# Optimization experiments

Hardware: AMD Instinct MI355X
Metric: run time of the kernel (lower is better)

The kernel has to match this reference:

```python
import jax, jax.numpy as jnp
import numpy as np

H = 16  # head_num


def setup_inputs() -> dict:
    key = jax.random.key(0)
    ks = jax.random.split(key, 16)
    B, N, D, DR = 4, 512, 1024, 128
    dk = D // H
    nrm = lambda i, shp, sc=1.0: jax.random.normal(ks[i], shp, jnp.float32) * sc
    inp = {
        "q": nrm(0, (B, N, D)),
        "k": nrm(1, (B, N, D)),
        "v": nrm(2, (B, N, D)),
        "r_k": nrm(3, (B, N, N, DR), 0.1),
        "r_v": nrm(4, (B, N, N, DR), 0.1),
        # learned params (Linear stored as [in, out] so y = x @ W + b)
        "Wq": nrm(5, (D, D), 1.0 / np.sqrt(D)), "bq": jnp.zeros((D,), jnp.float32),
        "Wk": nrm(6, (D, D), 1.0 / np.sqrt(D)), "bk": jnp.zeros((D,), jnp.float32),
        "Wv": nrm(7, (D, D), 1.0 / np.sqrt(D)), "bv": jnp.zeros((D,), jnp.float32),
        "Wrk": nrm(8, (DR, dk), 1.0 / np.sqrt(DR)), "brk": jnp.zeros((dk,), jnp.float32),
        "Wrv": nrm(9, (DR, dk), 1.0 / np.sqrt(DR)), "brv": jnp.zeros((dk,), jnp.float32),
        "Wo": nrm(10, (D, D), 1.0 / np.sqrt(D)), "bo": jnp.zeros((D,), jnp.float32),
    }
    return inp


def reference(q, k, v, r_k, r_v, Wq, bq, Wk, bk, Wv, bv, Wrk, brk, Wrv, brv, Wo, bo):
    B, N, D = q.shape
    dk = D // H
    scale = 1.0 / np.sqrt(dk).astype(np.float32)
    # relation projections ('concat' mode, rel_share=False): [B,N,N,d_rel] -> [B,N,N,d_k]
    rk = r_k @ Wrk + brk
    rv = r_v @ Wrv + brv

    def heads(x, W, b):  # [B,N,D] -> [B,H,N,dk]
        return (x @ W + b).reshape(B, N, H, dk).transpose(0, 2, 1, 3)

    qh = heads(q, Wq, bq)
    kh = heads(k, Wk, bk)
    vh = heads(v, Wv, bv)
    # score_1: standard scaled dot-product; score_2: relation bias per (query m, key n)
    score = jnp.einsum('bhmd,bhnd->bhmn', qh, kh) * scale \
          + jnp.einsum('bhmd,bmnd->bhmn', qh, rk)
    att = jax.nn.softmax(score, axis=-1)  # [B,H,N,N]
    # value_1: standard AV; value_2: relation-value combination
    val = jnp.einsum('bhmn,bhnd->bhmd', att, vh) \
        + jnp.einsum('bhmn,bmnd->bhmd', att, rv)
    out = val.transpose(0, 2, 1, 3).reshape(B, N, D) @ Wo + bo
    return out
```

## Files before the change

kernel.cpp:

```cpp
#include <hip/hip_runtime.h>
#include <hip/hip_bf16.h>
#include <hip/hip_fp16.h>
#include <stdint.h>


typedef __attribute__((ext_vector_type(4))) float f32x4;
typedef __attribute__((ext_vector_type(8))) short s16x8;

#define MFMA16(A, B, C) __builtin_amdgcn_mfma_f32_16x16x32_bf16(A, B, C, 0, 0, 0)

__device__ __forceinline__ uint16_t f2bf(float x) {
  uint32_t u = __float_as_uint(x);
  u += 0x7fffu + ((u >> 16) & 1u);
  return (uint16_t)(u >> 16);
}
__device__ __forceinline__ float bf2f(uint16_t u) {
  return __uint_as_float((uint32_t)u << 16);
}
__device__ __forceinline__ uint16_t f2h(float x) {
  __half h = __float2half_rn(x);
  return *reinterpret_cast<uint16_t*>(&h);
}
__device__ __forceinline__ float h2f(uint16_t u) {
  __half h = *reinterpret_cast<__half*>(&u);
  return __half2float(h);
}

__device__ __forceinline__ uint32_t cvtpk(float lo, float hi) {
  uint32_t r;
  asm("v_cvt_pk_bf16_f32 %0, %1, %2" : "=v"(r) : "v"(lo), "v"(hi));
  return r;
}

__device__ __forceinline__ s16x8 pack8(float4 a, float4 b) {
  union { uint32_t u[4]; s16x8 v; } r;
  r.u[0] = cvtpk(a.x, a.y);
  r.u[1] = cvtpk(a.z, a.w);
  r.u[2] = cvtpk(b.x, b.y);
  r.u[3] = cvtpk(b.z, b.w);
  return r.v;
}

__device__ __forceinline__ void gll16(const void* g, void* l) {
  __builtin_amdgcn_global_load_lds(
      (const __attribute__((address_space(1))) uint32_t*)(g),
      (__attribute__((address_space(3))) uint32_t*)(l), 16, 0, 0);
}

__global__ __launch_bounds__(256) void k_prep(
    const float* __restrict__ Wq, const float* __restrict__ Wk,
    const float* __restrict__ Wv, const float* __restrict__ Wo,
    const float* __restrict__ Wrk, const float* __restrict__ Wrv,
    uint16_t* __restrict__ WqT, uint16_t* __restrict__ WkT,
    uint16_t* __restrict__ WvT, uint16_t* __restrict__ WoT,
    uint16_t* __restrict__ WrkB, uint16_t* __restrict__ WrvT) {
  int z = blockIdx.y;
  int t = threadIdx.x;
  if (z == 4) {
    if (blockIdx.x == 0) {
      for (int i = t; i < 128 * 64; i += 256) WrkB[i] = f2bf(Wrk[i]);
      for (int i = t; i < 64 * 128; i += 256) {
        int d = i >> 7, r = i & 127;
        WrvT[i] = f2bf(Wrv[r * 64 + d]);
      }
    }
    return;
  }
  const float* W = (z == 0) ? Wq : (z == 1) ? Wk : (z == 2) ? Wv : Wo;
  uint16_t* O = (z == 0) ? WqT : (z == 1) ? WkT : (z == 2) ? WvT : WoT;
  int tk = (blockIdx.x >> 4) * 64;
  int tn = (blockIdx.x & 15) * 64;
  __shared__ float tile[64][65];
  {
    int kk = t >> 2, c0 = (t & 3) * 16;
    const float* src = W + (size_t)(tk + kk) * 1024 + tn + c0;
#pragma unroll
    for (int i = 0; i < 16; i += 4) {
      float4 v = *(const float4*)(src + i);
      tile[kk][c0 + i + 0] = v.x; tile[kk][c0 + i + 1] = v.y;
      tile[kk][c0 + i + 2] = v.z; tile[kk][c0 + i + 3] = v.w;
    }
  }
  __syncthreads();
  {
    int n_loc = t >> 2;
    int n = tn + n_loc;
#pragma unroll
    for (int cc = 0; cc < 2; ++cc) {
      int c = (t & 3) * 2 + cc;
      int csrc = c ^ (n & 7);
      s16x8 pk;
#pragma unroll
      for (int j = 0; j < 8; ++j) pk[j] = (short)f2bf(tile[csrc * 8 + j][n_loc]);
      *reinterpret_cast<s16x8*>(O + (size_t)n * 1024 + tk + c * 8) = pk;
    }
  }
}

__global__ __launch_bounds__(256) void k_projqkv(
    const float* __restrict__ Xq, const float* __restrict__ Xk,
    const float* __restrict__ Xv, const uint16_t* __restrict__ WTbase,
    const float* __restrict__ bq, const float* __restrict__ bk,
    const float* __restrict__ bv, uint16_t* __restrict__ outbase) {
  int mode = blockIdx.z;
  const float* X = (mode == 0) ? Xq : (mode == 1) ? Xk : Xv;
  const float* bias = (mode == 0) ? bq : (mode == 1) ? bk : bv;
  const uint16_t* WT = WTbase + (size_t)mode * (1u << 20);
  uint16_t* out = outbase + (size_t)mode * (2u << 20);

  __shared__ alignas(16) float Xs[128 * 64];
  __shared__ alignas(16) uint16_t Bs[128 * 64];
  int t = threadIdx.x, lane = t & 63, w = t >> 6, lr = lane & 15, lg = lane >> 4;
  int m0 = blockIdx.x * 128, n0 = blockIdx.y * 128;
  int wm = (w >> 1) * 64, wn = (w & 1) * 64;
  f32x4 acc[4][4];
#pragma unroll
  for (int i = 0; i < 4; ++i)
#pragma unroll
    for (int j = 0; j < 4; ++j) acc[i][j] = (f32x4){0.f, 0.f, 0.f, 0.f};
  for (int ko = 0; ko < 16; ++ko) {
    __syncthreads();
    {
#pragma unroll
      for (int i = 0; i < 8; ++i) {
        int u = i * 256 + t;
        int row = u >> 4, c16 = u & 15;
        int cs = c16 ^ (row & 15);
        gll16(X + (size_t)(m0 + row) * 1024 + ko * 64 + cs * 4, (char*)Xs + u * 16);
      }
#pragma unroll
      for (int i = 0; i < 4; ++i) {
        int u = i * 256 + t;
        int row = u >> 3, c2 = u & 7;
        gll16(WT + (size_t)(n0 + row) * 1024 + ko * 64 + c2 * 8, (char*)Bs + u * 16);
      }
    }
    __syncthreads();
#pragma unroll
    for (int kk = 0; kk < 2; ++kk) {
      s16x8 af[4], bf[4];
#pragma unroll
      for (int mt = 0; mt < 4; ++mt) {
        int row = wm + mt * 16 + lr;
        int c0 = kk * 8 + lg * 2;
        float4 v0 = *(const float4*)((const char*)Xs + row * 256 +
                                     ((c0 ^ (row & 15)) * 16));
        float4 v1 = *(const float4*)((const char*)Xs + row * 256 +
                                     (((c0 + 1) ^ (row & 15)) * 16));
        af[mt] = pack8(v0, v1);
      }
#pragma unroll
      for (int nt = 0; nt < 4; ++nt) {
        int row = wn + nt * 16 + lr;
        bf[nt] = *(const s16x8*)((const char*)Bs + row * 128 +
                                 (((kk * 32 + lg * 8) * 2) ^ ((row & 7) << 4)));
      }
#pragma unroll
      for (int mt = 0; mt < 4; ++mt)
#pragma unroll
        for (int nt = 0; nt < 4; ++nt)
          acc[mt][nt] = MFMA16(af[mt], bf[nt], acc[mt][nt]);
    }
  }
  float sc = (mode == 1) ? 0.125f : 1.0f;
#pragma unroll
  for (int mt = 0; mt < 4; ++mt) {
#pragma unroll
    for (int nt = 0; nt < 4; ++nt) {
      int col = n0 + wn + nt * 16 + lr;
      float bcol = bias[col];
      if (mode != 2) {
#pragma unroll
        for (int r = 0; r < 4; ++r) {
          int row = m0 + wm + mt * 16 + lg * 4 + r;
          out[(size_t)row * 1024 + col] = f2bf((acc[mt][nt][r] + bcol) * sc);
        }
      } else {
        int row0 = m0 + wm + mt * 16 + lg * 4;
        int b = row0 >> 9, n = row0 & 511;
        int h = col >> 6, d = col & 63;
        ushort4 pk;
        pk.x = f2bf(acc[mt][nt][0] + bcol);
        pk.y = f2bf(acc[mt][nt][1] + bcol);
        pk.z = f2bf(acc[mt][nt][2] + bcol);
        pk.w = f2bf(acc[mt][nt][3] + bcol);
        *reinterpret_cast<ushort4*>(out + ((size_t)(b * 16 + h) * 64 + d) * 512 + n) = pk;
      }
    }
  }
}

__global__ __launch_bounds__(256) void k_score1qt(
    const uint16_t* __restrict__ qh, const uint16_t* __restrict__ kh,
    const uint16_t* __restrict__ WrkB, uint16_t* __restrict__ S1,
    uint16_t* __restrict__ qt) {
  __shared__ alignas(16) uint16_t Qs[128 * 64];
  __shared__ alignas(16) uint16_t Ks[2][128 * 64];
  int t = threadIdx.x, lane = t & 63, w = t >> 6, lr = lane & 15, lg = lane >> 4;
  int b = blockIdx.z;
  if (blockIdx.x >= 4) {
    int slot = (blockIdx.x - 4) * 64 + blockIdx.y * 4 + b;
#pragma unroll
    for (int it = 0; it < 4; ++it) {
      int row0 = slot * 256 + it * 64 + w * 16;
      f32x4 acc[8];
#pragma unroll
      for (int i = 0; i < 8; ++i) acc[i] = (f32x4){0.f, 0.f, 0.f, 0.f};
      s16x8 af[2];
#pragma unroll
      for (int kk = 0; kk < 2; ++kk)
        af[kk] = *(const s16x8*)(qh + (size_t)(row0 + lr) * 64 + kk * 32 + lg * 8);
#pragma unroll
      for (int rt = 0; rt < 8; ++rt) {
#pragma unroll
        for (int kk = 0; kk < 2; ++kk) {
          s16x8 bf = *(const s16x8*)(WrkB + (size_t)(rt * 16 + lr) * 64 + kk * 32 + lg * 8);
          acc[rt] = MFMA16(af[kk], bf, acc[rt]);
        }
      }
#pragma unroll
      for (int rt = 0; rt < 8; ++rt)
#pragma unroll
        for (int r = 0; r < 4; ++r)
          qt[(size_t)(row0 + lg * 4 + r) * 128 + rt * 16 + lr] = f2bf(acc[rt][r]);
    }
    return;
  }
  int mt = blockIdx.x, h = blockIdx.y;
  int m0 = mt * 128;
  const char* qg = (const char*)(qh + (size_t)(b * 512 + m0) * 1024 + h * 64);
  const char* kg = (const char*)(kh + (size_t)b * 512 * 1024 + h * 64);
#pragma unroll
  for (int i = 0; i < 4; ++i) {
    int u = i * 256 + t;
    int row = u >> 3;
    int cs = (u & 7) ^ (row & 7);
    gll16(qg + (size_t)row * 2048 + cs * 16, (char*)Qs + u * 16);
    gll16(kg + (size_t)row * 2048 + cs * 16, (char*)Ks[0] + u * 16);
  }
  int wm = (w >> 1) * 64, wn = (w & 1) * 64;
  int hsw = (h & 7) << 3;
#pragma unroll
  for (int nt = 0; nt < 4; ++nt) {
    asm volatile("s_waitcnt vmcnt(0)" ::: "memory");
    __builtin_amdgcn_s_barrier();
    asm volatile("" ::: "memory");
    if (nt < 3) {
      const char* kgn = kg + (size_t)(nt + 1) * 128 * 2048;
#pragma unroll
      for (int i = 0; i < 4; ++i) {
        int u = i * 256 + t;
        int row = u >> 3;
        int cs = (u & 7) ^ (row & 7);
        gll16(kgn + (size_t)row * 2048 + cs * 16, (char*)Ks[(nt + 1) & 1] + u * 16);
      }
    }
    f32x4 acc[4][4];
#pragma unroll
    for (int i = 0; i < 4; ++i)
#pragma unroll
      for (int j = 0; j < 4; ++j) acc[i][j] = (f32x4){0.f, 0.f, 0.f, 0.f};
#pragma unroll
    for (int kk = 0; kk < 2; ++kk) {
      s16x8 af[4], bf[4];
#pragma unroll
      for (int mtt = 0; mtt < 4; ++mtt) {
        int row = wm + mtt * 16 + lr;
        af[mtt] = *(const s16x8*)((const char*)Qs + row * 128 +
                                  (((kk * 4 + lg) ^ (row & 7)) * 16));
      }
#pragma unroll
      for (int ntt = 0; ntt < 4; ++ntt) {
        int row = wn + ntt * 16 + lr;
        bf[ntt] = *(const s16x8*)((const char*)Ks[nt & 1] + row * 128 +
                                  (((kk * 4 + lg) ^ (row & 7)) * 16));
      }
#pragma unroll
      for (int mtt = 0; mtt < 4; ++mtt)
#pragma unroll
        for (int ntt = 0; ntt < 4; ++ntt)
          acc[mtt][ntt] = MFMA16(bf[ntt], af[mtt], acc[mtt][ntt]);
    }
#pragma unroll
    for (int mtt = 0; mtt < 4; ++mtt) {
#pragma unroll
      for (int ntt = 0; ntt < 4; ++ntt) {
        int m = b * 512 + m0 + wm + mtt * 16 + lr;
        int nsw = (nt * 128 + wn + ntt * 16 + lg * 4) ^ hsw;
        ushort4 u4;
        u4.x = f2h(acc[mtt][ntt][0]); u4.y = f2h(acc[mtt][ntt][1]);
        u4.z = f2h(acc[mtt][ntt][2]); u4.w = f2h(acc[mtt][ntt][3]);
        *(ushort4*)(S1 + (size_t)m * 8192 + h * 512 + nsw) = u4;
      }
    }
  }
}

#define RKSTEP(s)                                                              \
  {                                                                            \
    asm volatile("s_waitcnt vmcnt(%0)" ::                                      \
                 "i"(((s) < 2) ? 6 : (((s) < 31) ? 2 : 0)) : "memory");        \
    const char* bp_ = wpriv + ((s) & 1) * 2048 + lr * 128;                     \
    float4 v0_ = *(const float4*)(bp_ + (((lg * 2 + 0) ^ (lr & 7)) * 16));     \
    float4 v1_ = *(const float4*)(bp_ + (((lg * 2 + 1) ^ (lr & 7)) * 16));     \
    acc[(s) >> 2] = MFMA16(aqt[(s) & 3], pack8(v0_, v1_), acc[(s) >> 2]);      \
    if ((s) + 2 < 32) {                                                        \
      const int s2_ = (s) + 2;                                                 \
      const char* src_ = rkb + (size_t)((s2_ >> 2) * 64 + w * 16 + r_lo) * 512 \
                         + (s2_ & 3) * 128 + c16s * 16;                        \
      char* dst_ = wpriv + (s2_ & 1) * 2048 + lane * 16;                       \
      gll16(src_, dst_);                                                       \
      gll16(src_ + 8 * 512, dst_ + 1024);                                      \
    }                                                                          \
  }

#define RVI(c)                                                                 \
  { _Pragma("unroll")                                                          \
    for (int i_ = 0; i_ < 2; ++i_) {                                           \
      int u_ = i_ * 64 + lane;                                                 \
      gll16(rvb + (size_t)(((c) >> 1) * 32 + (u_ >> 2)) * 512 + w * 128 +      \
                ((c) & 1) * 64 + (u_ & 3) * 16,                                \
            wpriv + ((c) & 1) * 2048 + u_ * 16);                               \
    } }

#define RVC(c, accv)                                                           \
  {                                                                            \
    s16x8 a_ = *(const s16x8*)((const char*)att_lds + lr * 1024 +              \
        (((uint32_t)(((c) >> 1) * 64 + lg * 16)) ^ ((uint32_t)(lr & 7) << 4)));\
    const float* vb_ = (const float*)(wpriv + ((c) & 1) * 2048);               \
    union { uint32_t u[4]; s16x8 v; } bb_;                                     \
    _Pragma("unroll")                                                          \
    for (int i = 0; i < 4; ++i)                                                \
      bb_.u[i] = cvtpk(vb_[(lg * 8 + 2 * i) * 16 + lr],                        \
                       vb_[(lg * 8 + 2 * i + 1) * 16 + lr]);                   \
    accv = MFMA16(a_, bb_.v, accv);                                            \
  }

__global__ __launch_bounds__(256, 4) void k_s2v2(
    const uint16_t* __restrict__ qt, const float* __restrict__ rk,
    const float* __restrict__ rv, uint16_t* SATT,
    const uint16_t* __restrict__ WrvT, const float* __restrict__ brv,
    uint16_t* __restrict__ V2) {
  int bm = blockIdx.x;
  int t = threadIdx.x, lane = t & 63, w = t >> 6, lr = lane & 15, lg = lane >> 4;
  __shared__ alignas(16) char stream_lds[16384];
  __shared__ alignas(16) uint16_t att_lds[16 * 512];
  __shared__ alignas(16) uint16_t arv_lds[16 * 128];
  __shared__ float red[2][16][4];
  char* wpriv = stream_lds + w * 4096;
  const int r_lo = lane >> 3;
  const int c16s = (lane & 7) ^ r_lo;

  s16x8 aqt[4];
#pragma unroll
  for (int kk = 0; kk < 4; ++kk)
    aqt[kk] = *(const s16x8*)(qt + ((size_t)bm * 16 + lr) * 128 + kk * 32 + lg * 8);

  const char* rkb = (const char*)(rk + (size_t)bm * 65536);
#pragma unroll
  for (int s2 = 0; s2 < 2; ++s2) {
    const char* src_ = rkb + (size_t)(w * 16 + r_lo) * 512 + s2 * 128 + c16s * 16;
    char* dst_ = wpriv + s2 * 2048 + lane * 16;
    gll16(src_, dst_);
    gll16(src_ + 8 * 512, dst_ + 1024);
  }
  const char* s1g = (const char*)(SATT + (size_t)bm * 8192);
#pragma unroll
  for (int i = 0; i < 4; ++i)
    gll16(s1g + i * 4096 + t * 16, (char*)att_lds + i * 4096 + t * 16);

  f32x4 acc[8];
#pragma unroll
  for (int j = 0; j < 8; ++j) acc[j] = (f32x4){0.f, 0.f, 0.f, 0.f};

  RKSTEP(0)  RKSTEP(1)  RKSTEP(2)  RKSTEP(3)  RKSTEP(4)  RKSTEP(5)  RKSTEP(6)  RKSTEP(7)
  RKSTEP(8)  RKSTEP(9)  RKSTEP(10) RKSTEP(11) RKSTEP(12) RKSTEP(13) RKSTEP(14) RKSTEP(15)
  RKSTEP(16) RKSTEP(17) RKSTEP(18) RKSTEP(19) RKSTEP(20) RKSTEP(21) RKSTEP(22) RKSTEP(23)
  RKSTEP(24) RKSTEP(25) RKSTEP(26) RKSTEP(27) RKSTEP(28) RKSTEP(29) RKSTEP(30) RKSTEP(31)

  __syncthreads();

  const char* rvb = (const char*)(rv + (size_t)bm * 65536);
  RVI(0) RVI(1)

#pragma unroll
  for (int idx = 0; idx < 8; ++idx) {
#pragma unroll
    for (int r = 0; r < 4; ++r) {
      int h = lg * 4 + r;
      int n = idx * 64 + w * 16 + lr;
      uint16_t s1v = *(const uint16_t*)((const char*)att_lds + h * 1024 +
                     (((uint32_t)n * 2) ^ ((uint32_t)(h & 7) << 4)));
      acc[idx][r] += h2f(s1v);
    }
  }

  float mrow[4], inv[4];
#pragma unroll
  for (int r = 0; r < 4; ++r) {
    float mx = acc[0][r];
#pragma unroll
    for (int j = 1; j < 8; ++j) mx = fmaxf(mx, acc[j][r]);
#pragma unroll
    for (int off = 1; off < 16; off <<= 1) mx = fmaxf(mx, __shfl_xor(mx, off, 64));
    mrow[r] = mx;
  }
  if (lr == 0) {
#pragma unroll
    for (int r = 0; r < 4; ++r) red[0][lg * 4 + r][w] = mrow[r];
  }
  __syncthreads();
#pragma unroll
  for (int r = 0; r < 4; ++r) {
    const float* p = red[0][lg * 4 + r];
    mrow[r] = fmaxf(fmaxf(p[0], p[1]), fmaxf(p[2], p[3]));
  }
#pragma unroll
  for (int r = 0; r < 4; ++r) {
    float s = 0.f;
#pragma unroll
    for (int j = 0; j < 8; ++j) {
      float pj = __expf(acc[j][r] - mrow[r]);
      acc[j][r] = pj;
      s += pj;
    }
#pragma unroll
    for (int off = 1; off < 16; off <<= 1) s += __shfl_xor(s, off, 64);
    inv[r] = s;
  }
  if (lr == 0) {
#pragma unroll
    for (int r = 0; r < 4; ++r) red[1][lg * 4 + r][w] = inv[r];
  }
  __syncthreads();
#pragma unroll
  for (int r = 0; r < 4; ++r) {
    const float* p = red[1][lg * 4 + r];
    inv[r] = 1.f / (p[0] + p[1] + p[2] + p[3]);
  }
#pragma unroll
  for (int r = 0; r < 4; ++r) {
    int h = lg * 4 + r;
#pragma unroll
    for (int idx = 0; idx < 8; ++idx) {
      int n = idx * 64 + w * 16 + lr;
      uint32_t off = (uint32_t)h * 1024 + (((uint32_t)n * 2) ^ ((uint32_t)(h & 7) << 4));
      *(uint16_t*)((char*)att_lds + off) = f2bf(acc[idx][r] * inv[r]);
    }
  }
  __syncthreads();

  f32x4 arv0 = (f32x4){0.f, 0.f, 0.f, 0.f}, arv1 = arv0;
#pragma unroll 1
  for (int cp = 0; cp < 14; ++cp) {
    asm volatile("s_waitcnt vmcnt(2)" ::: "memory");
    RVC(2 * cp, arv0)
    RVI(2 * cp + 2)
    asm volatile("s_waitcnt vmcnt(2)" ::: "memory");
    RVC(2 * cp + 1, arv1)
    RVI(2 * cp + 3)
  }
  asm volatile("s_waitcnt vmcnt(2)" ::: "memory");
  RVC(28, arv0)
  RVI(30)
  asm volatile("s_waitcnt vmcnt(2)" ::: "memory");
  RVC(29, arv1)
  RVI(31)
  asm volatile("s_waitcnt vmcnt(2)" ::: "memory");
  RVC(30, arv0)
  asm volatile("s_waitcnt vmcnt(0)" ::: "memory");
  RVC(31, arv1)

#pragma unroll
  for (int r = 0; r < 4; ++r) {
    int h = lg * 4 + r;
    uint32_t rc0 = (uint32_t)(w * 32 + lr) * 2;
    uint32_t rc1 = (uint32_t)(w * 32 + 16 + lr) * 2;
    *(uint16_t*)((char*)arv_lds + h * 256 + (rc0 ^ ((uint32_t)(h & 7) << 4))) = f2bf(arv0[r]);
    *(uint16_t*)((char*)arv_lds + h * 256 + (rc1 ^ ((uint32_t)(h & 7) << 4))) = f2bf(arv1[r]);
  }
  __syncthreads();
  f32x4 vacc = (f32x4){0.f, 0.f, 0.f, 0.f};
#pragma unroll
  for (int kk = 0; kk < 4; ++kk) {
    uint32_t rb = (uint32_t)(kk * 32 + lg * 8) * 2;
    s16x8 a = *(const s16x8*)((const char*)arv_lds + lr * 256 +
                              (rb ^ ((uint32_t)(lr & 7) << 4)));
    s16x8 bfw = *(const s16x8*)(WrvT + (size_t)(w * 16 + lr) * 128 + kk * 32 + lg * 8);
    vacc = MFMA16(a, bfw, vacc);
  }
  float bias = brv[w * 16 + lr];
#pragma unroll
  for (int r = 0; r < 4; ++r)
    V2[(size_t)bm * 1024 + (lg * 4 + r) * 64 + w * 16 + lr] = f2bf(vacc[r] + bias);

#pragma unroll
  for (int i = 0; i < 4; ++i) {
    s16x8 vv = *(const s16x8*)((const char*)att_lds + i * 4096 + t * 16);
    *(s16x8*)((char*)SATT + (size_t)bm * 16384 + i * 4096 + t * 16) = vv;
  }
}

__global__ __launch_bounds__(256, 4) void k_val1(
    const uint16_t* __restrict__ vhT, const uint16_t* __restrict__ ATT,
    const uint16_t* __restrict__ V2, uint16_t* __restrict__ VALB) {
  int t = threadIdx.x, lane = t & 63, w = t >> 6, lr = lane & 15, lg = lane >> 4;
  int mt = blockIdx.x, h = blockIdx.y, b = blockIdx.z;
  int mb = mt * 64 + w * 16;
  const uint16_t* vrow = vhT + ((size_t)((b * 16 + h) * 64) + lr) * 512 + lg * 8;
  const uint16_t* arow = ATT + (size_t)(b * 512 + mb + lr) * 8192 + h * 512;
  f32x4 acc[4];
#pragma unroll
  for (int j = 0; j < 4; ++j) acc[j] = (f32x4){0.f, 0.f, 0.f, 0.f};
#pragma unroll 4
  for (int kk = 0; kk < 16; ++kk) {
    int nsw = (kk * 32 + lg * 8) ^ ((h & 7) << 3);
    s16x8 a0 = *(const s16x8*)(arow + nsw);
#pragma unroll
    for (int dt = 0; dt < 4; ++dt) {
      s16x8 vf = *(const s16x8*)(vrow + (size_t)dt * 16 * 512 + kk * 32);
      acc[dt] = MFMA16(vf, a0, acc[dt]);
    }
  }
#pragma unroll
  for (int dt = 0; dt < 4; ++dt) {
    size_t adr = (size_t)(b * 512 + mb + lr) * 1024 + h * 64 + dt * 16 + lg * 4;
    ushort4 v2v = *(const ushort4*)(V2 + adr);
    ushort4 o;
    o.x = f2bf(acc[dt][0] + bf2f(v2v.x));
    o.y = f2bf(acc[dt][1] + bf2f(v2v.y));
    o.z = f2bf(acc[dt][2] + bf2f(v2v.z));
    o.w = f2bf(acc[dt][3] + bf2f(v2v.w));
    *(ushort4*)(VALB + adr) = o;
  }
}

__global__ __launch_bounds__(256) void k_out(
    const uint16_t* __restrict__ A, const uint16_t* __restrict__ WT,
    const float* __restrict__ bias, float* __restrict__ out) {
  __shared__ alignas(16) uint16_t As[128 * 64];
  __shared__ alignas(16) uint16_t Bs[128 * 64];
  int t = threadIdx.x, lane = t & 63, w = t >> 6, lr = lane & 15, lg = lane >> 4;
  int m0 = blockIdx.x * 128, n0 = blockIdx.y * 128;
  int wm = (w >> 1) * 64, wn = (w & 1) * 64;
  f32x4 acc[4][4];
#pragma unroll
  for (int i = 0; i < 4; ++i)
#pragma unroll
    for (int j = 0; j < 4; ++j) acc[i][j] = (f32x4){0.f, 0.f, 0.f, 0.f};
  for (int ko = 0; ko < 16; ++ko) {
    __syncthreads();
    {
#pragma unroll
      for (int i = 0; i < 4; ++i) {
        int u = i * 256 + t;
        int row = u >> 3, c2 = u & 7;
        int cs = c2 ^ (row & 7);
        gll16(A + (size_t)(m0 + row) * 1024 + ko * 64 + cs * 8, (char*)As + u * 16);
        gll16(WT + (size_t)(n0 + row) * 1024 + ko * 64 + c2 * 8, (char*)Bs + u * 16);
      }
    }
    __syncthreads();
#pragma unroll
    for (int kk = 0; kk < 2; ++kk) {
      s16x8 af[4], bf[4];
#pragma unroll
      for (int mt = 0; mt < 4; ++mt) {
        int row = wm + mt * 16 + lr;
        af[mt] = *(const s16x8*)((const char*)As + row * 128 +
                                 (((kk * 32 + lg * 8) * 2) ^ ((row & 7) << 4)));
      }
#pragma unroll
      for (int nt = 0; nt < 4; ++nt) {
        int row = wn + nt * 16 + lr;
        bf[nt] = *(const s16x8*)((const char*)Bs + row * 128 +
                                 (((kk * 32 + lg * 8) * 2) ^ ((row & 7) << 4)));
      }
#pragma unroll
      for (int mt = 0; mt < 4; ++mt)
#pragma unroll
        for (int nt = 0; nt < 4; ++nt)
          acc[mt][nt] = MFMA16(af[mt], bf[nt], acc[mt][nt]);
    }
  }
#pragma unroll
  for (int mt = 0; mt < 4; ++mt) {
#pragma unroll
    for (int nt = 0; nt < 4; ++nt) {
      int col = n0 + wn + nt * 16 + lr;
      float bcol = bias[col];
#pragma unroll
      for (int r = 0; r < 4; ++r) {
        int row = m0 + wm + mt * 16 + lg * 4 + r;
        out[(size_t)row * 1024 + col] = acc[mt][nt][r] + bcol;
      }
    }
  }
}

extern "C" void kernel_launch(void* const* d_in, const int* in_sizes, int n_in,
                              void* d_out, int out_size, void* d_ws, size_t ws_size,
                              hipStream_t stream) {
  const float* q   = (const float*)d_in[0];
  const float* k_  = (const float*)d_in[1];
  const float* v   = (const float*)d_in[2];
  const float* r_k = (const float*)d_in[3];
  const float* r_v = (const float*)d_in[4];
  const float* Wq  = (const float*)d_in[5];
  const float* bq  = (const float*)d_in[6];
  const float* Wk  = (const float*)d_in[7];
  const float* bk  = (const float*)d_in[8];
  const float* Wv  = (const float*)d_in[9];
  const float* bv  = (const float*)d_in[10];
  const float* Wrk = (const float*)d_in[11];
  const float* Wrv = (const float*)d_in[13];
  const float* brv = (const float*)d_in[14];
  const float* Wo  = (const float*)d_in[15];
  const float* bo  = (const float*)d_in[16];
  (void)in_sizes; (void)n_in; (void)out_size;

  char* ws = (char*)d_ws;
  uint16_t* WqT  = (uint16_t*)(ws + (size_t)(0));
  uint16_t* WkT  = (uint16_t*)(ws + (size_t)(2u << 20));
  uint16_t* WvT  = (uint16_t*)(ws + (size_t)(4u << 20));
  uint16_t* WoT  = (uint16_t*)(ws + (size_t)(6u << 20));
  uint16_t* WrkB = (uint16_t*)(ws + (size_t)(8u << 20));
  uint16_t* WrvT = (uint16_t*)(ws + (size_t)(8u << 20) + (64u << 10));
  uint16_t* QH   = (uint16_t*)(ws + (size_t)(16u << 20));
  uint16_t* KH   = (uint16_t*)(ws + (size_t)(20u << 20));
  uint16_t* VHT  = (uint16_t*)(ws + (size_t)(24u << 20));
  uint16_t* QT   = (uint16_t*)(ws + (size_t)(28u << 20));
  uint16_t* VALB = (uint16_t*)(ws + (size_t)(36u << 20));
  uint16_t* V2   = (uint16_t*)(ws + (size_t)(16u << 20));
  uint16_t* SATT = (uint16_t*)(ws + (size_t)(40u << 20));
  if (ws_size < (size_t)(74u << 20)) return;

  dim3 blk(256, 1, 1);
  k_prep<<<dim3(256, 5, 1), blk, 0, stream>>>(Wq, Wk, Wv, Wo, Wrk, Wrv,
                                              WqT, WkT, WvT, WoT, WrkB, WrvT);
  k_projqkv<<<dim3(16, 8, 3), blk, 0, stream>>>(q, k_, v, WqT, bq, bk, bv, QH);
  k_score1qt<<<dim3(6, 16, 4), blk, 0, stream>>>(QH, KH, WrkB, SATT, QT);
  k_s2v2<<<dim3(2048, 1, 1), blk, 0, stream>>>(QT, r_k, r_v, SATT, WrvT, brv, V2);
  k_val1<<<dim3(8, 16, 4), blk, 0, stream>>>(VHT, SATT, V2, VALB);
  k_out<<<dim3(16, 8, 1), blk, 0, stream>>>(VALB, WoT, bo, (float*)d_out);
}
```

Before: 341.4 us.

## Store attention in fragment-major layout and load rk without XOR swizzle

Changes the rk streaming in k_s2v2 so each lane fetches the exact 16-byte chunks it later reads, making LDS reads linear by lane instead of swizzled. Rewrites the normalized attention written to LDS and global SATT into an MFMA-fragment-ordered layout, so RVC and k_val1 read contiguous 16-byte slots per lane with no XOR address math. The layout change must match every producer and consumer of SATT. The new global pattern may reduce coalescing of the rk loads, and the scattered 2-byte LDS writes may cause bank conflicts.

```diff
diff --git a/kernel.cpp b/kernel.cpp
--- a/kernel.cpp
+++ b/kernel.cpp
@@ -300,17 +300,17 @@
   {                                                                            \
     asm volatile("s_waitcnt vmcnt(%0)" ::                                      \
                  "i"(((s) < 2) ? 6 : (((s) < 31) ? 2 : 0)) : "memory");        \
-    const char* bp_ = wpriv + ((s) & 1) * 2048 + lr * 128;                     \
-    float4 v0_ = *(const float4*)(bp_ + (((lg * 2 + 0) ^ (lr & 7)) * 16));     \
-    float4 v1_ = *(const float4*)(bp_ + (((lg * 2 + 1) ^ (lr & 7)) * 16));     \
+    const char* bp_ = wpriv + ((s) & 1) * 2048;                                \
+    float4 v0_ = *(const float4*)(bp_ + lane * 16);                            \
+    float4 v1_ = *(const float4*)(bp_ + 1024 + lane * 16);                     \
     acc[(s) >> 2] = MFMA16(aqt[(s) & 3], pack8(v0_, v1_), acc[(s) >> 2]);      \
     if ((s) + 2 < 32) {                                                        \
       const int s2_ = (s) + 2;                                                 \
-      const char* src_ = rkb + (size_t)((s2_ >> 2) * 64 + w * 16 + r_lo) * 512 \
-                         + (s2_ & 3) * 128 + c16s * 16;                        \
+      const char* rb_ = rkb + (size_t)((s2_ >> 2) * 64 + w * 16 + (lane & 15)) \
+                        * 512 + (s2_ & 3) * 128;                               \
       char* dst_ = wpriv + (s2_ & 1) * 2048 + lane * 16;                       \
-      gll16(src_, dst_);                                                       \
-      gll16(src_ + 8 * 512, dst_ + 1024);                                      \
+      gll16(rb_ + (2 * (lane >> 4)) * 16, dst_);                               \
+      gll16(rb_ + (2 * (lane >> 4) + 1) * 16, dst_ + 1024);                    \
     }                                                                          \
   }
 
@@ -325,8 +325,8 @@
 
 #define RVC(c, accv)                                                           \
   {                                                                            \
-    s16x8 a_ = *(const s16x8*)((const char*)att_lds + lr * 1024 +              \
-        (((uint32_t)(((c) >> 1) * 64 + lg * 16)) ^ ((uint32_t)(lr & 7) << 4)));\
+    s16x8 a_ = *(const s16x8*)((const char*)att_lds +                          \
+                               (((c) >> 1) * 64 + lane) * 16);                 \
     const float* vb_ = (const float*)(wpriv + ((c) & 1) * 2048);               \
     union { uint32_t u[4]; s16x8 v; } bb_;                                     \
     _Pragma("unroll")                                                          \
@@ -348,8 +348,6 @@
   __shared__ alignas(16) uint16_t arv_lds[16 * 128];
   __shared__ float red[2][16][4];
   char* wpriv = stream_lds + w * 4096;
-  const int r_lo = lane >> 3;
-  const int c16s = (lane & 7) ^ r_lo;
 
   s16x8 aqt[4];
 #pragma unroll
@@ -359,10 +357,10 @@
   const char* rkb = (const char*)(rk + (size_t)bm * 65536);
 #pragma unroll
   for (int s2 = 0; s2 < 2; ++s2) {
-    const char* src_ = rkb + (size_t)(w * 16 + r_lo) * 512 + s2 * 128 + c16s * 16;
+    const char* rb_ = rkb + (size_t)(w * 16 + (lane & 15)) * 512 + s2 * 128;
     char* dst_ = wpriv + s2 * 2048 + lane * 16;
-    gll16(src_, dst_);
-    gll16(src_ + 8 * 512, dst_ + 1024);
+    gll16(rb_ + (2 * (lane >> 4)) * 16, dst_);
+    gll16(rb_ + (2 * (lane >> 4) + 1) * 16, dst_ + 1024);
   }
   const char* s1g = (const char*)(SATT + (size_t)bm * 8192);
 #pragma unroll
@@ -443,9 +441,9 @@
     int h = lg * 4 + r;
 #pragma unroll
     for (int idx = 0; idx < 8; ++idx) {
-      int n = idx * 64 + w * 16 + lr;
-      uint32_t off = (uint32_t)h * 1024 + (((uint32_t)n * 2) ^ ((uint32_t)(h & 7) << 4));
-      *(uint16_t*)((char*)att_lds + off) = f2bf(acc[idx][r] * inv[r]);
+      int slot = (idx * 2 + (w >> 1)) * 64 + ((w & 1) * 2 + (lr >> 3)) * 16 + h;
+      *(uint16_t*)((char*)att_lds + slot * 16 + (lr & 7) * 2) =
+          f2bf(acc[idx][r] * inv[r]);
     }
   }
   __syncthreads();
@@ -508,14 +506,13 @@
   int mt = blockIdx.x, h = blockIdx.y, b = blockIdx.z;
   int mb = mt * 64 + w * 16;
   const uint16_t* vrow = vhT + ((size_t)((b * 16 + h) * 64) + lr) * 512 + lg * 8;
-  const uint16_t* arow = ATT + (size_t)(b * 512 + mb + lr) * 8192 + h * 512;
+  const uint16_t* arow = ATT + (size_t)(b * 512 + mb + lr) * 8192 + lg * 128 + h * 8;
   f32x4 acc[4];
 #pragma unroll
   for (int j = 0; j < 4; ++j) acc[j] = (f32x4){0.f, 0.f, 0.f, 0.f};
 #pragma unroll 4
   for (int kk = 0; kk < 16; ++kk) {
-    int nsw = (kk * 32 + lg * 8) ^ ((h & 7) << 3);
-    s16x8 a0 = *(const s16x8*)(arow + nsw);
+    s16x8 a0 = *(const s16x8*)(arow + kk * 512);
 #pragma unroll
     for (int dt = 0; dt < 4; ++dt) {
       s16x8 vf = *(const s16x8*)(vrow + (size_t)dt * 16 * 512 + kk * 32);
```

Result: slower. 349.6 us (+2.4%).
